# Performance work log

Hardware: AMD Instinct MI355X
Metric: run time of the kernel (lower is better)

Reference implementation:

```python
import jax, jax.numpy as jnp
import numpy as np

BIT_WIDTH = 8
N_LEVELS = 1 << BIT_WIDTH          # 256
NUM_Q = 256                        # num_quantized_values
THD_NEG = -(1 << (BIT_WIDTH - 1))  # -128
THD_POS = (1 << (BIT_WIDTH - 1)) - 1  # 127
TAU = 1.0                          # gumbel-softmax temperature
SHAPE = (512, 512)


def setup_inputs() -> dict:
    key = jax.random.key(0)
    k1, k2 = jax.random.split(key)
    # quantized integer values in [thd_neg, thd_pos]
    quantized_values = jax.random.randint(k1, SHAPE, THD_NEG, THD_POS + 1, dtype=jnp.int32)
    # identity init: logits[i, i % n_levels] = 10.0
    rows = jnp.arange(NUM_Q)
    encoding_logits = jnp.zeros((NUM_Q, N_LEVELS), jnp.float32).at[rows, rows % N_LEVELS].set(10.0)
    # precomputed gumbel noise (torch F.gumbel_softmax samples this internally)
    gumbel_noise = jax.random.gumbel(k2, SHAPE + (N_LEVELS,), dtype=jnp.float32)
    return {"quantized_values": quantized_values,
            "encoding_logits": encoding_logits,
            "gumbel_noise": gumbel_noise}


def reference(quantized_values, encoding_logits, gumbel_noise):
    # _value_to_indices: identity mapping is contiguous over [-128,127], so the
    # dict lookup + nearest-mapped-value fallback reduces exactly to a clamp.
    idx = jnp.clip(quantized_values, THD_NEG, THD_POS) - THD_NEG  # [*] int
    logits = encoding_logits[idx]                                  # [*, n_levels] gather
    # straight-through: hard argmax code + (soft - stop_grad(soft))
    hard_codes = jnp.argmax(logits, axis=-1).astype(jnp.float32)   # [*]
    soft_codes = jax.nn.softmax((logits + gumbel_noise) / TAU, axis=-1)  # [*, n_levels]
    # torch broadcast: hard [*] + soft [*, n_levels] -> [*, n_levels]
    codes = hard_codes[..., None] + soft_codes - jax.lax.stop_gradient(soft_codes)
    return codes
```

## Files before the change

kernel.cpp:

```cpp
#include <hip/hip_runtime.h>
#include <hip/hip_bf16.h>


#define N_LEVELS 256
#define THD_NEG (-128)

__global__ __launch_bounds__(256) void olm_argmax_table(
    const float* __restrict__ logits, float* __restrict__ table) {
    int r = threadIdx.x;
    const float* row = logits + (size_t)r * N_LEVELS;
    float best = row[0];
    int bi = 0;
#pragma unroll 8
    for (int k = 1; k < N_LEVELS; ++k) {
        float v = row[k];
        if (v > best) { best = v; bi = k; }
    }
    table[r] = (float)bi;
}

__global__ __launch_bounds__(256) void olm_write_codes(
    const int* __restrict__ q, const float* __restrict__ table,
    float* __restrict__ out, int nrows) {
    __shared__ float tab[N_LEVELS];
    tab[threadIdx.x] = table[threadIdx.x];
    __syncthreads();

    int gid  = blockIdx.x * blockDim.x + threadIdx.x;
    int lane = gid & 63;
    int row0 = gid >> 6;
    int row_stride = (gridDim.x * blockDim.x) >> 6;

    for (int row = row0; row < nrows; row += row_stride) {
        int qv = q[row];
        qv = min(127, max(-128, qv));
        float v = tab[qv - THD_NEG];
        float4 v4 = {v, v, v, v};
        reinterpret_cast<float4*>(out + (size_t)row * N_LEVELS)[lane] = v4;
    }
}

__global__ __launch_bounds__(256) void olm_write_codes_fused(
    const int* __restrict__ q, const float* __restrict__ logits,
    float* __restrict__ out, int nrows) {
    __shared__ float tab[N_LEVELS];
    {
        const float* row = logits + (size_t)threadIdx.x * N_LEVELS;
        float best = row[0];
        int bi = 0;
        for (int k = 1; k < N_LEVELS; ++k) {
            float v = row[k];
            if (v > best) { best = v; bi = k; }
        }
        tab[threadIdx.x] = (float)bi;
    }
    __syncthreads();

    int gid  = blockIdx.x * blockDim.x + threadIdx.x;
    int lane = gid & 63;
    int row0 = gid >> 6;
    int row_stride = (gridDim.x * blockDim.x) >> 6;

    for (int row = row0; row < nrows; row += row_stride) {
        int qv = q[row];
        qv = min(127, max(-128, qv));
        float v = tab[qv - THD_NEG];
        float4 v4 = {v, v, v, v};
        reinterpret_cast<float4*>(out + (size_t)row * N_LEVELS)[lane] = v4;
    }
}

extern "C" void kernel_launch(void* const* d_in, const int* in_sizes, int n_in,
                              void* d_out, int out_size, void* d_ws, size_t ws_size,
                              hipStream_t stream) {
    const int*   q      = (const int*)d_in[0];
    const float* logits = (const float*)d_in[1];
    float* out = (float*)d_out;

    const int nrows = in_sizes[0];
    const int block = 256;
    int rows_per_block = block / 64;
    int blocks_needed = (nrows + rows_per_block - 1) / rows_per_block;
    int grid = blocks_needed < 4096 ? blocks_needed : 4096;

    if (ws_size >= N_LEVELS * sizeof(float)) {
        float* table = (float*)d_ws;
        olm_argmax_table<<<1, 256, 0, stream>>>(logits, table);
        olm_write_codes<<<grid, block, 0, stream>>>(q, table, out, nrows);
    } else {
        olm_write_codes_fused<<<grid, block, 0, stream>>>(q, logits, out, nrows);
    }
}
```

Baseline: 404.8 us.

## Parallelize argmax table with wave reductions and batch row writes per wave

The argmax table is now built with one wavefront per logits row, using a vectorized load and a shuffle reduction across 64 lanes, spread over 64 blocks instead of one serial thread per row. The write kernel gives each wave 64 rows: one coalesced load of q, a broadcast of each row's value by shuffle, and nontemporal float4 stores replacing the grid-stride loop. This cuts the serial table latency and the per-row index loads, and keeps the large output stream from polluting the cache. The fused fallback path for a missing workspace is removed, so the code now assumes the workspace is always present.

```diff
diff --git a/kernel.cpp b/kernel.cpp
--- a/kernel.cpp
+++ b/kernel.cpp
@@ -2,71 +2,55 @@
 #include <hip/hip_bf16.h>
 
 
-#define N_LEVELS 256
-#define THD_NEG (-128)
+#define NLV 256
 
-__global__ __launch_bounds__(256) void olm_argmax_table(
+typedef float f32x4 __attribute__((ext_vector_type(4)));
+
+__global__ __launch_bounds__(256) void olm_table(
     const float* __restrict__ logits, float* __restrict__ table) {
-    int r = threadIdx.x;
-    const float* row = logits + (size_t)r * N_LEVELS;
-    float best = row[0];
-    int bi = 0;
-#pragma unroll 8
-    for (int k = 1; k < N_LEVELS; ++k) {
-        float v = row[k];
-        if (v > best) { best = v; bi = k; }
+    int wid  = (blockIdx.x * blockDim.x + threadIdx.x) >> 6;
+    int lane = threadIdx.x & 63;
+    if (wid >= NLV) return;
+
+    f32x4 v4 = reinterpret_cast<const f32x4*>(logits + (size_t)wid * NLV)[lane];
+    float best = v4.x; int bi = lane * 4;
+    if (v4.y > best) { best = v4.y; bi = lane * 4 + 1; }
+    if (v4.z > best) { best = v4.z; bi = lane * 4 + 2; }
+    if (v4.w > best) { best = v4.w; bi = lane * 4 + 3; }
+
+    for (int off = 32; off > 0; off >>= 1) {
+        float ob = __shfl_xor(best, off, 64);
+        int   oi = __shfl_xor(bi,   off, 64);
+        if (ob > best || (ob == best && oi < bi)) { best = ob; bi = oi; }
     }
-    table[r] = (float)bi;
+    if (lane == 0) table[wid] = (float)bi;
 }
 
-__global__ __launch_bounds__(256) void olm_write_codes(
+__global__ __launch_bounds__(256) void olm_write(
     const int* __restrict__ q, const float* __restrict__ table,
     float* __restrict__ out, int nrows) {
-    __shared__ float tab[N_LEVELS];
+    __shared__ float tab[NLV];
     tab[threadIdx.x] = table[threadIdx.x];
     __syncthreads();
 
-    int gid  = blockIdx.x * blockDim.x + threadIdx.x;
-    int lane = gid & 63;
-    int row0 = gid >> 6;
-    int row_stride = (gridDim.x * blockDim.x) >> 6;
+    int lane = threadIdx.x & 63;
+    int wid  = (blockIdx.x * blockDim.x + threadIdx.x) >> 6;
+    int base = wid * 64;
+    if (base >= nrows) return;
+    int n = nrows - base; if (n > 64) n = 64;
 
-    for (int row = row0; row < nrows; row += row_stride) {
-        int qv = q[row];
-        qv = min(127, max(-128, qv));
-        float v = tab[qv - THD_NEG];
-        float4 v4 = {v, v, v, v};
-        reinterpret_cast<float4*>(out + (size_t)row * N_LEVELS)[lane] = v4;
-    }
-}
+    int qi = base + (lane < n ? lane : n - 1);
+    int qv = q[qi];
+    qv = min(127, max(-128, qv)) + 128;
+    float myv = tab[qv];
 
-__global__ __launch_bounds__(256) void olm_write_codes_fused(
-    const int* __restrict__ q, const float* __restrict__ logits,
-    float* __restrict__ out, int nrows) {
-    __shared__ float tab[N_LEVELS];
-    {
-        const float* row = logits + (size_t)threadIdx.x * N_LEVELS;
-        float best = row[0];
-        int bi = 0;
-        for (int k = 1; k < N_LEVELS; ++k) {
-            float v = row[k];
-            if (v > best) { best = v; bi = k; }
-        }
-        tab[threadIdx.x] = (float)bi;
-    }
-    __syncthreads();
-
-    int gid  = blockIdx.x * blockDim.x + threadIdx.x;
-    int lane = gid & 63;
-    int row0 = gid >> 6;
-    int row_stride = (gridDim.x * blockDim.x) >> 6;
-
-    for (int row = row0; row < nrows; row += row_stride) {
-        int qv = q[row];
-        qv = min(127, max(-128, qv));
-        float v = tab[qv - THD_NEG];
-        float4 v4 = {v, v, v, v};
-        reinterpret_cast<float4*>(out + (size_t)row * N_LEVELS)[lane] = v4;
+    f32x4* orow = reinterpret_cast<f32x4*>(out + (size_t)base * NLV) + lane;
+#pragma unroll 4
+    for (int r = 0; r < n; ++r) {
+        float v = __shfl(myv, r, 64);
+        f32x4 v4 = {v, v, v, v};
+        __builtin_nontemporal_store(v4, orow);
+        orow += NLV / 4;
     }
 }
 
@@ -75,19 +59,14 @@
                               hipStream_t stream) {
     const int*   q      = (const int*)d_in[0];
     const float* logits = (const float*)d_in[1];
-    float* out = (float*)d_out;
+    float* out   = (float*)d_out;
+    float* table = (float*)d_ws;
 
     const int nrows = in_sizes[0];
-    const int block = 256;
-    int rows_per_block = block / 64;
-    int blocks_needed = (nrows + rows_per_block - 1) / rows_per_block;
-    int grid = blocks_needed < 4096 ? blocks_needed : 4096;
 
-    if (ws_size >= N_LEVELS * sizeof(float)) {
-        float* table = (float*)d_ws;
-        olm_argmax_table<<<1, 256, 0, stream>>>(logits, table);
-        olm_write_codes<<<grid, block, 0, stream>>>(q, table, out, nrows);
-    } else {
-        olm_write_codes_fused<<<grid, block, 0, stream>>>(q, logits, out, nrows);
-    }
+    olm_table<<<(NLV * 64 + 255) / 256, 256, 0, stream>>>(logits, table);
+
+    int waves  = (nrows + 63) / 64;
+    int blocks = (waves * 64 + 255) / 256;
+    olm_write<<<blocks, 256, 0, stream>>>(q, table, out, nrows);
 }
```

Measured after the change: 383.0 us. -5.4%, faster.
